# Kernel tuning notes

Measured on AMD Instinct MI355X. Metric: run time of the kernel, lower is better.

Reference implementation:

```python
import jax, jax.numpy as jnp
import numpy as np

HID = 1024
INTER = 4096
RDIM = 128          # expert_retrieval_size
HEADS = 4
NUM_EXPERTS = 16384
NUM_KEYS = 128      # sqrt(NUM_EXPERTS)
TOPK = 8            # num_cdmoe_experts_per_head
B, T = 2, 2048


def setup_inputs() -> dict:
    key = jax.random.key(0)
    ks = jax.random.split(key, 8)
    s = lambda fan_in: 1.0 / np.sqrt(fan_in)
    return {
        "hidden_states": jax.random.normal(ks[0], (B, T, HID), jnp.float32),
        "Wq": jax.random.normal(ks[1], (HEADS * RDIM, HID), jnp.float32) * s(HID),
        "keys": jax.random.normal(ks[2], (HEADS, NUM_KEYS, 2, RDIM // 2), jnp.float32) * s(RDIM // 2),
        "down_embed": jax.random.normal(ks[3], (NUM_EXPERTS, HID), jnp.float32) * 0.02,
        "up_embed": jax.random.normal(ks[4], (NUM_EXPERTS, HID), jnp.float32) * 0.02,
        "Wg": jax.random.normal(ks[5], (INTER, HID), jnp.float32) * s(HID),
        "Wu": jax.random.normal(ks[6], (INTER, HID), jnp.float32) * s(HID),
        "Wd": jax.random.normal(ks[7], (HID, INTER), jnp.float32) * s(INTER),
    }


def reference(hidden_states, Wq, keys, down_embed, up_embed, Wg, Wu, Wd):
    b, t, _ = hidden_states.shape
    # product-key retrieval
    q = hidden_states @ Wq.T                                   # [b,t,h*rdim]
    q = q.reshape(b, t, 2, HEADS, RDIM // 2)                   # [b,t,2,h,n]
    q = jnp.transpose(q, (2, 0, 1, 3, 4))                      # [2,b,t,h,n]
    sim = jnp.einsum('pbthn,hkpn->pbthk', q, keys)             # [2,b,t,h,K]
    sx, ix = jax.lax.top_k(sim[0], TOPK)                       # [b,t,h,k]
    sy, iy = jax.lax.top_k(sim[1], TOPK)
    all_scores = (sx[..., :, None] + sy[..., None, :]).reshape(b, t, HEADS, TOPK * TOPK)
    all_indices = (ix[..., :, None] * NUM_KEYS + iy[..., None, :]).reshape(b, t, HEADS, TOPK * TOPK)
    scores, pk = jax.lax.top_k(all_scores, TOPK)               # [b,t,h,k]
    indices = jnp.take_along_axis(all_indices, pk, axis=-1)    # [b,t,h,k]
    # gather expert embeddings and combine
    down = down_embed[indices]                                 # [b,t,h,k,d]
    up = up_embed[indices]                                     # [b,t,h,k,d]
    w = jnp.einsum('btd,bthkd->bthk', hidden_states, down)
    w = jax.nn.silu(w) * jax.nn.softmax(scores, axis=-1)
    experts_states = jnp.einsum('bthk,bthkd->btd', w, up)
    # dense MLP
    mlp = (jax.nn.silu(hidden_states @ Wg.T) * (hidden_states @ Wu.T)) @ Wd.T
    return mlp + experts_states
```

## Files before the change

kernel.cpp:

```cpp
#include <hip/hip_runtime.h>
#include <hip/hip_fp8.h>

#define NTOK 4096
#define HID 1024
#define QDIM 512
#define HEADS 4
#define NKEYS 128
#define TOPK 8
#define INTERDIM 4096

typedef __bf16 bf16x8 __attribute__((ext_vector_type(8)));
typedef __bf16 bf16x4 __attribute__((ext_vector_type(4)));
typedef float f32x4 __attribute__((ext_vector_type(4)));
typedef float f32x2 __attribute__((ext_vector_type(2)));

__device__ __forceinline__ float siluf(float x) { return x / (1.f + __expf(-x)); }
__device__ __forceinline__ unsigned sortable(float f) {
  unsigned u = __float_as_uint(f);
  return (u & 0x80000000u) ? ~u : (u | 0x80000000u);
}
__device__ __forceinline__ float bfl(unsigned u) { return __uint_as_float(u << 16); }
__device__ __forceinline__ float bfh(unsigned u) { return __uint_as_float(u & 0xFFFF0000u); }

__device__ __forceinline__ unsigned fp8x4_enc(float4 v) {
#if __has_builtin(__builtin_amdgcn_cvt_pk_fp8_f32)
  unsigned u = __builtin_amdgcn_cvt_pk_fp8_f32(v.x, v.y, 0, false);
  u = __builtin_amdgcn_cvt_pk_fp8_f32(v.z, v.w, u, true);
  return u;
#else
  __hip_fp8_e4m3 a(v.x), b(v.y), c(v.z), d(v.w);
  return (unsigned)a.__x | ((unsigned)b.__x << 8) | ((unsigned)c.__x << 16) | ((unsigned)d.__x << 24);
#endif
}
__device__ __forceinline__ void fp8x4_dec(unsigned u, float* o) {
#if __has_builtin(__builtin_amdgcn_cvt_pk_f32_fp8)
  f32x2 lo = __builtin_amdgcn_cvt_pk_f32_fp8(u, false);
  f32x2 hi = __builtin_amdgcn_cvt_pk_f32_fp8(u, true);
  o[0] = lo[0]; o[1] = lo[1]; o[2] = hi[0]; o[3] = hi[1];
#else
#pragma unroll
  for (int j = 0; j < 4; ++j) {
    const unsigned b = (u >> (8 * j)) & 0xFF;
    const unsigned e = (b >> 3) & 15, m = b & 7;
    float v = e ? __uint_as_float(((e + 120) << 23) | (m << 20)) : (float)m * 0x1p-9f;
    o[j] = (b & 0x80) ? -v : v;
  }
#endif
}

#define GLD_LDS16(g, l)                                                                   \
  __builtin_amdgcn_global_load_lds(                                                      \
      (const __attribute__((address_space(1))) unsigned int*)(g),                        \
      (__attribute__((address_space(3))) unsigned int*)(l), 16, 0, 0)

__device__ __forceinline__ void cast_one_f4(const float* __restrict__ src,
                                            __bf16* __restrict__ dst, int i)
{
  const float4 v = ((const float4*)src)[i];
  bf16x4 o;
  o[0] = (__bf16)v.x; o[1] = (__bf16)v.y; o[2] = (__bf16)v.z; o[3] = (__bf16)v.w;
  ((bf16x4*)dst)[i] = o;
}

__global__ __launch_bounds__(256) void cast5_kernel(
    const float* __restrict__ hs, const float* __restrict__ wq,
    const float* __restrict__ wg, const float* __restrict__ wu,
    const float* __restrict__ wd,
    __bf16* __restrict__ hs_o, __bf16* __restrict__ wq_o,
    __bf16* __restrict__ wg_o, __bf16* __restrict__ wu_o,
    __bf16* __restrict__ wd_o)
{
  int b = blockIdx.x;
  const float* src; __bf16* dst;
  if      (b < 4096)  { src = hs; dst = hs_o; }
  else if (b < 4608)  { src = wq; dst = wq_o; b -= 4096; }
  else if (b < 8704)  { src = wg; dst = wg_o; b -= 4608; }
  else if (b < 12800) { src = wu; dst = wu_o; b -= 8704; }
  else                { src = wd; dst = wd_o; b -= 12800; }
  cast_one_f4(src, dst, b * 256 + threadIdx.x);
}

__global__ __launch_bounds__(256) void cast2_kernel(
    const float* __restrict__ dwe, const float* __restrict__ upe,
    unsigned* __restrict__ dwe_o, unsigned* __restrict__ upe_o)
{
  int b = blockIdx.x;
  const float* src; unsigned* dst;
  if (b < 16384) { src = dwe; dst = dwe_o; }
  else           { src = upe; dst = upe_o; b -= 16384; }
  const int i = b * 256 + threadIdx.x;
  dst[i] = fp8x4_enc(((const float4*)src)[i]);
}

__global__ __launch_bounds__(256) void cast_keys_kernel(const float* __restrict__ keys,
                                                        __bf16* __restrict__ kbf)
{
  const int i = blockIdx.x * 256 + threadIdx.x;
  const int n = i & 63, p = (i >> 6) & 1, k = (i >> 7) & 127, h = (i >> 14) & 3;
  kbf[(((size_t)(p * 4 + h) * NKEYS) + k) * 64 + n] = (__bf16)keys[i];
}

template<bool DUAL, bool OUT_BF16>
__global__ __launch_bounds__(512) void gemm_mfma(
    const __bf16* __restrict__ A, const __bf16* __restrict__ B0,
    const __bf16* __restrict__ B1, void* __restrict__ Cv, __bf16* __restrict__ Cv1,
    int M, int N, int K, int LD, int BW, int BH, int NRX)
{
  __shared__ __attribute__((aligned(16))) __bf16 As [128 * 32];
  __shared__ __attribute__((aligned(16))) __bf16 Bs0[128 * 32];
  __shared__ __attribute__((aligned(16))) __bf16 Bs1[DUAL ? 128 * 32 : 8];

  const int bid = blockIdx.y * gridDim.x + blockIdx.x;
  const int xcd = bid & 7, idx = bid >> 3;
  const int rx = (xcd % NRX) * BW;
  const int ry = (xcd / NRX) * BH;
  const int bx = rx + idx % BW;
  const int by = ry + idx / BW;

  const int kz = blockIdx.z * K;

  const int tid  = threadIdx.x;
  const int wave = tid >> 6;
  const int lane = tid & 63;
  const int m0 = by * 128;
  const int n0 = bx * 128;
  const int wr = wave >> 2, wc = wave & 3;
  const int lhi = lane >> 4, llo = lane & 15;

  f32x4 acc0[4][2] = {};
  f32x4 acc1[4][2] = {};

  const int r0 = tid >> 2, col0 = (tid & 3) * 8;
  const __bf16* Ag  = A  + kz + (size_t)(m0 + r0) * LD + col0;
  const __bf16* B0g = B0 + kz + (size_t)(n0 + r0) * LD + col0;
  const __bf16* B1g = DUAL ? (B1 + kz + (size_t)(n0 + r0) * LD + col0) : nullptr;
  __bf16* ldsA  = &As [(size_t)wave * 512];
  __bf16* ldsB0 = &Bs0[(size_t)wave * 512];
  __bf16* ldsB1 = &Bs1[(size_t)wave * 512];

  for (int k0 = 0; k0 < K; k0 += 32) {
    GLD_LDS16(Ag  + k0, ldsA);
    GLD_LDS16(B0g + k0, ldsB0);
    if constexpr (DUAL)
      GLD_LDS16(B1g + k0, ldsB1);
    __syncthreads();

    bf16x8 afr[4], bfr0[2], bfr1[2];
#pragma unroll
    for (int mi = 0; mi < 4; ++mi)
      afr[mi] = *(const bf16x8*)&As[(wr * 64 + mi * 16 + llo) * 32 + lhi * 8];
#pragma unroll
    for (int nj = 0; nj < 2; ++nj)
      bfr0[nj] = *(const bf16x8*)&Bs0[(wc * 32 + nj * 16 + llo) * 32 + lhi * 8];
    if constexpr (DUAL) {
#pragma unroll
      for (int nj = 0; nj < 2; ++nj)
        bfr1[nj] = *(const bf16x8*)&Bs1[(wc * 32 + nj * 16 + llo) * 32 + lhi * 8];
    }
#pragma unroll
    for (int mi = 0; mi < 4; ++mi)
#pragma unroll
      for (int nj = 0; nj < 2; ++nj) {
        acc0[mi][nj] = __builtin_amdgcn_mfma_f32_16x16x32_bf16(afr[mi], bfr0[nj], acc0[mi][nj], 0, 0, 0);
        if constexpr (DUAL)
          acc1[mi][nj] = __builtin_amdgcn_mfma_f32_16x16x32_bf16(afr[mi], bfr1[nj], acc1[mi][nj], 0, 0, 0);
      }
    __syncthreads();
  }

#pragma unroll
  for (int mi = 0; mi < 4; ++mi)
#pragma unroll
    for (int nj = 0; nj < 2; ++nj)
#pragma unroll
      for (int r = 0; r < 4; ++r) {
        const int row = m0 + wr * 64 + mi * 16 + lhi * 4 + r;
        const int col = n0 + wc * 32 + nj * 16 + llo;
        float v = acc0[mi][nj][r];
        if constexpr (DUAL) v = siluf(v) * acc1[mi][nj][r];
        if constexpr (OUT_BF16) {
          ((__bf16*)Cv)[(size_t)row * N + col] = (__bf16)v;
        } else {
          if (blockIdx.z == 0) ((float*)Cv)[(size_t)row * N + col] = v;
          else Cv1[((size_t)(blockIdx.z - 1) * M + row) * N + col] = (__bf16)v;
        }
      }
}

__global__ __launch_bounds__(256) void sims_gemm(
    const __bf16* __restrict__ Qbf,
    const __bf16* __restrict__ Kbf,
    float* __restrict__ S)
{
  __shared__ __attribute__((aligned(16))) __bf16 As[128 * 32];
  __shared__ __attribute__((aligned(16))) __bf16 Bs[128 * 32];

  const int z = blockIdx.y;
  const int p = z >> 2, h = z & 3;
  const __bf16* A = Qbf + p * 256 + h * 64;
  const __bf16* B = Kbf + (size_t)z * NKEYS * 64;
  float* C = S + (size_t)z * NTOK * NKEYS;

  const int tid  = threadIdx.x;
  const int wave = tid >> 6;
  const int lane = tid & 63;
  const int m0 = blockIdx.x * 128;
  const int wr = wave >> 1, wc = wave & 1;
  const int lhi = lane >> 4, llo = lane & 15;

  f32x4 acc[4][4] = {};

  const int c0 = tid, c1 = 256 + tid;
  const int r0 = c0 >> 2, col0 = (c0 & 3) * 8;
  const int r1 = c1 >> 2, col1 = (c1 & 3) * 8;
  __bf16* ldsA0 = &As[(wave * 64) * 8];
  __bf16* ldsA1 = &As[(256 + wave * 64) * 8];
  __bf16* ldsB0 = &Bs[(wave * 64) * 8];
  __bf16* ldsB1 = &Bs[(256 + wave * 64) * 8];

  for (int k0 = 0; k0 < 64; k0 += 32) {
    GLD_LDS16(A + (size_t)(m0 + r0) * 512 + k0 + col0, ldsA0);
    GLD_LDS16(A + (size_t)(m0 + r1) * 512 + k0 + col1, ldsA1);
    GLD_LDS16(B + (size_t)r0 * 64 + k0 + col0, ldsB0);
    GLD_LDS16(B + (size_t)r1 * 64 + k0 + col1, ldsB1);
    __syncthreads();

    bf16x8 afr[4], bfr[4];
#pragma unroll
    for (int mi = 0; mi < 4; ++mi)
      afr[mi] = *(const bf16x8*)&As[(wr * 64 + mi * 16 + llo) * 32 + lhi * 8];
#pragma unroll
    for (int nj = 0; nj < 4; ++nj)
      bfr[nj] = *(const bf16x8*)&Bs[(wc * 64 + nj * 16 + llo) * 32 + lhi * 8];
#pragma unroll
    for (int mi = 0; mi < 4; ++mi)
#pragma unroll
      for (int nj = 0; nj < 4; ++nj)
        acc[mi][nj] = __builtin_amdgcn_mfma_f32_16x16x32_bf16(afr[mi], bfr[nj], acc[mi][nj], 0, 0, 0);
    __syncthreads();
  }

#pragma unroll
  for (int mi = 0; mi < 4; ++mi)
#pragma unroll
    for (int nj = 0; nj < 4; ++nj)
#pragma unroll
      for (int r = 0; r < 4; ++r) {
        const int row = m0 + wr * 64 + mi * 16 + lhi * 4 + r;
        const int col = wc * 64 + nj * 16 + llo;
        C[(size_t)row * NKEYS + col] = acc[mi][nj][r];
      }
}

__global__ __launch_bounds__(256) void topk_kernel(
    const float* __restrict__ S,
    int* __restrict__ out_idx,
    float* __restrict__ out_prob)
{
  const int g = blockIdx.x;
  const int h = blockIdx.y;
  const int t = threadIdx.x;
  const int tok0 = g * 16;

  __shared__ float    sims  [16][2][128];
  __shared__ unsigned packed[16][2][128];
  __shared__ unsigned cmax  [16][2][8];
  __shared__ int      cnt   [16][2];
  __shared__ unsigned char surv[16][2][128];
  __shared__ float    stv   [16][2][8];
  __shared__ unsigned char sti[16][2][8];
  __shared__ unsigned cnd   [16][64];

  const int ltok = t >> 4, j0 = (t & 15) * 8;
  unsigned pk[2][8];
#pragma unroll
  for (int p = 0; p < 2; ++p) {
    const float* src = S + (((size_t)(p * 4 + h) * NTOK) + tok0 + ltok) * NKEYS + j0;
    const float4 a = ((const float4*)src)[0];
    const float4 b = ((const float4*)src)[1];
    float v[8] = {a.x, a.y, a.z, a.w, b.x, b.y, b.z, b.w};
#pragma unroll
    for (int e = 0; e < 8; ++e) {
      const unsigned u = (sortable(v[e]) & 0xFFFFFF80u) | (unsigned)(127 - (j0 + e));
      sims  [ltok][p][j0 + e] = v[e];
      packed[ltok][p][j0 + e] = u;
      pk[p][e] = u;
    }
  }
  if (t < 32) cnt[t >> 1][t & 1] = 0;
  __syncthreads();

  {
    const int ctok = t >> 4, cp = (t >> 3) & 1, c = t & 7;
    const uint4* q = (const uint4*)&packed[ctok][cp][c * 16];
    unsigned m = 0;
#pragma unroll
    for (int r = 0; r < 4; ++r) {
      const uint4 u = q[r];
      m = max(m, max(max(u.x, u.y), max(u.z, u.w)));
    }
    cmax[ctok][cp][c] = m;
  }
  __syncthreads();

#pragma unroll
  for (int p = 0; p < 2; ++p) {
    const uint4* cm = (const uint4*)&cmax[ltok][p][0];
    const uint4 ca = cm[0], cb = cm[1];
    const unsigned t0 = min(min(min(ca.x, ca.y), min(ca.z, ca.w)),
                            min(min(cb.x, cb.y), min(cb.z, cb.w)));
#pragma unroll
    for (int e = 0; e < 8; ++e) {
      if (pk[p][e] >= t0) {
        const int s = atomicAdd(&cnt[ltok][p], 1);
        surv[ltok][p][s] = (unsigned char)(j0 + e);
      }
    }
  }
  __syncthreads();

  {
    const int gid = t >> 3, lane8 = t & 7;
    const int stok = gid >> 1, sp = gid & 1;
    const int n = cnt[stok][sp];
    const uint4* row = (const uint4*)&packed[stok][sp][0];
    for (int s = lane8; s < n; s += 8) {
      const int j = surv[stok][sp][s];
      const unsigned mypk = packed[stok][sp][j];
      int rk = 0;
#pragma unroll 8
      for (int q4 = 0; q4 < 32; ++q4) {
        const uint4 u = row[q4];
        rk += (u.x > mypk) + (u.y > mypk) + (u.z > mypk) + (u.w > mypk);
      }
      if (rk < TOPK) {
        stv[stok][sp][rk] = sims[stok][sp][j];
        sti[stok][sp][rk] = (unsigned char)j;
      }
    }
  }
  __syncthreads();

  const int w = t >> 6, l = t & 63;
  for (int round = 0; round < 4; ++round) {
    const int tok = w * 4 + round;
    const int ci = l >> 3, cj = l & 7;
    const float cv = stv[tok][0][ci] + stv[tok][1][cj];
    const unsigned cpk = (sortable(cv) & 0xFFFFFFC0u) | (unsigned)(63 - l);
    cnd[tok][l] = cpk;
    __syncthreads();
    int rk = 0;
    const uint4* row = (const uint4*)&cnd[tok][0];
#pragma unroll
    for (int q4 = 0; q4 < 16; ++q4) {
      const uint4 u = row[q4];
      rk += (u.x > cpk) + (u.y > cpk) + (u.z > cpk) + (u.w > cpk);
    }
    float mx = cv;
#pragma unroll
    for (int off = 32; off; off >>= 1) mx = fmaxf(mx, __shfl_xor(mx, off));
    const float e = (rk < TOPK) ? __expf(cv - mx) : 0.f;
    float sum = e;
#pragma unroll
    for (int off = 32; off; off >>= 1) sum += __shfl_xor(sum, off);
    if (rk < TOPK) {
      const int o = ((tok0 + tok) * HEADS + h) * TOPK + rk;
      out_idx [o] = (int)sti[tok][0][ci] * NKEYS + (int)sti[tok][1][cj];
      out_prob[o] = e / sum;
    }
  }
}

__device__ __forceinline__ float dotf8(const float4* h, uint4 d)
{
  float o[16];
  fp8x4_dec(d.x, o);  fp8x4_dec(d.y, o + 4);
  fp8x4_dec(d.z, o + 8); fp8x4_dec(d.w, o + 12);
  float s = 0.f;
#pragma unroll
  for (int q = 0; q < 4; ++q)
    s += h[q].x * o[4*q] + h[q].y * o[4*q+1] + h[q].z * o[4*q+2] + h[q].w * o[4*q+3];
  return s;
}

template<int NPART>
__global__ __launch_bounds__(256) void expert_kernel(
    const float* __restrict__ hs,
    const unsigned char* __restrict__ down_e,
    const unsigned char* __restrict__ up_e,
    const int* __restrict__ idx,
    const float* __restrict__ prob,
    const __bf16* __restrict__ parts,
    float* __restrict__ out)
{
  const int token = blockIdx.x;
  const int t = threadIdx.x, w = t >> 6, l = t & 63;
  __shared__ float4 sred[4][256];

  const float4* hrow = (const float4*)(hs + (size_t)token * HID);
  float4 h[4];
#pragma unroll
  for (int q = 0; q < 4; ++q) h[q] = hrow[4 * l + q];
  float acc[16] = {};

  const int*   tidx  = idx  + token * 32 + w * 8;
  const float* tprob = prob + token * 32 + w * 8;

#pragma unroll
  for (int e = 0; e < 8; e += 2) {
    const int   ex0 = tidx[e],  ex1 = tidx[e + 1];
    const float pr0 = tprob[e], pr1 = tprob[e + 1];
    const uint4 d0 = ((const uint4*)(down_e + (size_t)ex0 * HID))[l];
    const uint4 d1 = ((const uint4*)(down_e + (size_t)ex1 * HID))[l];
    const uint4 u0 = ((const uint4*)(up_e   + (size_t)ex0 * HID))[l];
    const uint4 u1 = ((const uint4*)(up_e   + (size_t)ex1 * HID))[l];

    float part0 = dotf8(h, d0);
    float part1 = dotf8(h, d1);
#pragma unroll
    for (int off = 32; off; off >>= 1) {
      part0 += __shfl_xor(part0, off);
      part1 += __shfl_xor(part1, off);
    }
    const float w0 = siluf(part0) * pr0;
    const float w1 = siluf(part1) * pr1;

    float o0[16], o1[16];
    fp8x4_dec(u0.x, o0); fp8x4_dec(u0.y, o0 + 4); fp8x4_dec(u0.z, o0 + 8); fp8x4_dec(u0.w, o0 + 12);
    fp8x4_dec(u1.x, o1); fp8x4_dec(u1.y, o1 + 4); fp8x4_dec(u1.z, o1 + 8); fp8x4_dec(u1.w, o1 + 12);
#pragma unroll
    for (int j = 0; j < 16; ++j) acc[j] += w0 * o0[j] + w1 * o1[j];
  }
#pragma unroll
  for (int q = 0; q < 4; ++q)
    sred[w][4 * l + q] = make_float4(acc[4*q], acc[4*q+1], acc[4*q+2], acc[4*q+3]);
  __syncthreads();

  const float4 r0 = sred[0][t], r1 = sred[1][t], r2 = sred[2][t], r3 = sred[3][t];
  float4* o = (float4*)(out + (size_t)token * HID);
  float4 cur = o[t];
  if constexpr (NPART > 0) {
#pragma unroll
    for (int q = 0; q < NPART; ++q) {
      const uint2 pb = ((const uint2*)(parts + ((size_t)q * NTOK + token) * HID))[t];
      cur.x += bfl(pb.x); cur.y += bfh(pb.x);
      cur.z += bfl(pb.y); cur.w += bfh(pb.y);
    }
  }
  cur.x += r0.x + r1.x + r2.x + r3.x;
  cur.y += r0.y + r1.y + r2.y + r3.y;
  cur.z += r0.z + r1.z + r2.z + r3.z;
  cur.w += r0.w + r1.w + r2.w + r3.w;
  o[t] = cur;
}

extern "C" void kernel_launch(void* const* d_in, const int* in_sizes, int n_in,
                              void* d_out, int out_size, void* d_ws, size_t ws_size,
                              hipStream_t stream)
{
  const float* hs   = (const float*)d_in[0];
  const float* Wq   = (const float*)d_in[1];
  const float* keys = (const float*)d_in[2];
  const float* dwe  = (const float*)d_in[3];
  const float* upe  = (const float*)d_in[4];
  const float* Wg   = (const float*)d_in[5];
  const float* Wu   = (const float*)d_in[6];
  const float* Wd   = (const float*)d_in[7];
  float* out = (float*)d_out;

  __bf16* qbf     = (__bf16*)d_ws;
  __bf16* kbf     = qbf + (size_t)NTOK * QDIM;
  int*    idxb    = (int*)(kbf + 8 * NKEYS * 64);
  float*  probb   = (float*)(idxb + NTOK * HEADS * TOPK);
  __bf16* hs_bf   = (__bf16*)(probb + NTOK * HEADS * TOPK);
  __bf16* wq_bf   = hs_bf + (size_t)NTOK * HID;
  __bf16* wg_bf   = wq_bf + (size_t)QDIM * HID;
  __bf16* wu_bf   = wg_bf + (size_t)INTERDIM * HID;
  __bf16* wd_bf   = wu_bf + (size_t)INTERDIM * HID;
  __bf16* interbf = wd_bf + (size_t)HID * INTERDIM;
  __bf16* parts   = interbf + (size_t)NTOK * INTERDIM;
  float*  simsb   = (float*)interbf;
  unsigned char* dwe_f8 = (unsigned char*)interbf;
  unsigned char* upe_f8 = (unsigned char*)hs_bf;

  const size_t base  = (size_t)((char*)parts - (char*)d_ws);
  const size_t psz   = (size_t)NTOK * HID * sizeof(__bf16);
  int nsplit = 1;
  if      (ws_size >= base + 3 * psz) nsplit = 4;
  else if (ws_size >= base + 1 * psz) nsplit = 2;

  cast5_kernel<<<16896, 256, 0, stream>>>(hs, Wq, Wg, Wu, Wd,
                                          hs_bf, wq_bf, wg_bf, wu_bf, wd_bf);
  cast_keys_kernel<<<256, 256, 0, stream>>>(keys, kbf);

  gemm_mfma<false, true><<<dim3(QDIM / 128, NTOK / 128), 512, 0, stream>>>(
      hs_bf, wq_bf, nullptr, qbf, nullptr, NTOK, QDIM, HID, HID, 4, 4, 1);

  sims_gemm<<<dim3(NTOK / 128, 8), 256, 0, stream>>>(qbf, kbf, simsb);
  topk_kernel<<<dim3(NTOK / 16, HEADS), 256, 0, stream>>>(simsb, idxb, probb);

  gemm_mfma<true, true><<<dim3(INTERDIM / 128, NTOK / 128), 512, 0, stream>>>(
      hs_bf, wg_bf, wu_bf, interbf, nullptr, NTOK, INTERDIM, HID, HID, 8, 16, 4);

  gemm_mfma<false, false><<<dim3(HID / 128, NTOK / 128, nsplit), 512, 0, stream>>>(
      interbf, wd_bf, nullptr, out, parts, NTOK, HID, INTERDIM / nsplit, INTERDIM, 8, 4, 1);

  cast2_kernel<<<32768, 256, 0, stream>>>(dwe, upe, (unsigned*)dwe_f8, (unsigned*)upe_f8);
  if (nsplit == 4)
    expert_kernel<3><<<NTOK, 256, 0, stream>>>(hs, dwe_f8, upe_f8, idxb, probb, parts, out);
  else if (nsplit == 2)
    expert_kernel<1><<<NTOK, 256, 0, stream>>>(hs, dwe_f8, upe_f8, idxb, probb, parts, out);
  else
    expert_kernel<0><<<NTOK, 256, 0, stream>>>(hs, dwe_f8, upe_f8, idxb, probb, nullptr, out);
}
```

Measured before the change: 287.6 us.

## Fold product keys into query weights and compute similarities in one GEMM

Precomputes WK = keys·Wq per (half, head, key) so that similarity scores come directly from hidden_states @ WK^T as a single 4096x1024x1024 GEMM. This replaces the separate query projection GEMM, the bf16 query buffer round trip, the key cast kernel and the small sims GEMM. The top-k kernel now reads scores in a token-major layout. The trade-off is a larger GEMM (N=1024 instead of 512 plus a tiny second GEMM) and a different rounding order, since the combined weights are rounded to bf16.

```diff
diff --git a/kernel.cpp b/kernel.cpp
--- a/kernel.cpp
+++ b/kernel.cpp
@@ -92,12 +92,31 @@
   dst[i] = fp8x4_enc(((const float4*)src)[i]);
 }
 
-__global__ __launch_bounds__(256) void cast_keys_kernel(const float* __restrict__ keys,
-                                                        __bf16* __restrict__ kbf)
-{
-  const int i = blockIdx.x * 256 + threadIdx.x;
-  const int n = i & 63, p = (i >> 6) & 1, k = (i >> 7) & 127, h = (i >> 14) & 3;
-  kbf[(((size_t)(p * 4 + h) * NKEYS) + k) * 64 + n] = (__bf16)keys[i];
+__global__ __launch_bounds__(256) void wk_kernel(
+    const float* __restrict__ keys,
+    const float* __restrict__ wq,
+    __bf16* __restrict__ wk)
+{
+  const int zk = blockIdx.x;
+  const int z = zk >> 7, k = zk & 127;
+  const int p = z >> 2, h = z & 3;
+  __shared__ float kv[64];
+  if (threadIdx.x < 64)
+    kv[threadIdx.x] = keys[(((size_t)(h * NKEYS + k) * 2) + p) * 64 + threadIdx.x];
+  __syncthreads();
+
+  const int d0 = threadIdx.x * 4;
+  const float* wrow = wq + (size_t)(p * 256 + h * 64) * HID + d0;
+  float acc[4] = {};
+#pragma unroll 8
+  for (int n = 0; n < 64; ++n) {
+    const float kn = kv[n];
+    const float4 w = *(const float4*)(wrow + (size_t)n * HID);
+    acc[0] += kn * w.x; acc[1] += kn * w.y; acc[2] += kn * w.z; acc[3] += kn * w.w;
+  }
+  bf16x4 o;
+  o[0] = (__bf16)acc[0]; o[1] = (__bf16)acc[1]; o[2] = (__bf16)acc[2]; o[3] = (__bf16)acc[3];
+  ((bf16x4*)(wk + (size_t)zk * HID))[threadIdx.x] = o;
 }
 
 template<bool DUAL, bool OUT_BF16>
@@ -187,71 +206,6 @@
       }
 }
 
-__global__ __launch_bounds__(256) void sims_gemm(
-    const __bf16* __restrict__ Qbf,
-    const __bf16* __restrict__ Kbf,
-    float* __restrict__ S)
-{
-  __shared__ __attribute__((aligned(16))) __bf16 As[128 * 32];
-  __shared__ __attribute__((aligned(16))) __bf16 Bs[128 * 32];
-
-  const int z = blockIdx.y;
-  const int p = z >> 2, h = z & 3;
-  const __bf16* A = Qbf + p * 256 + h * 64;
-  const __bf16* B = Kbf + (size_t)z * NKEYS * 64;
-  float* C = S + (size_t)z * NTOK * NKEYS;
-
-  const int tid  = threadIdx.x;
-  const int wave = tid >> 6;
-  const int lane = tid & 63;
-  const int m0 = blockIdx.x * 128;
-  const int wr = wave >> 1, wc = wave & 1;
-  const int lhi = lane >> 4, llo = lane & 15;
-
-  f32x4 acc[4][4] = {};
-
-  const int c0 = tid, c1 = 256 + tid;
-  const int r0 = c0 >> 2, col0 = (c0 & 3) * 8;
-  const int r1 = c1 >> 2, col1 = (c1 & 3) * 8;
-  __bf16* ldsA0 = &As[(wave * 64) * 8];
-  __bf16* ldsA1 = &As[(256 + wave * 64) * 8];
-  __bf16* ldsB0 = &Bs[(wave * 64) * 8];
-  __bf16* ldsB1 = &Bs[(256 + wave * 64) * 8];
-
-  for (int k0 = 0; k0 < 64; k0 += 32) {
-    GLD_LDS16(A + (size_t)(m0 + r0) * 512 + k0 + col0, ldsA0);
-    GLD_LDS16(A + (size_t)(m0 + r1) * 512 + k0 + col1, ldsA1);
-    GLD_LDS16(B + (size_t)r0 * 64 + k0 + col0, ldsB0);
-    GLD_LDS16(B + (size_t)r1 * 64 + k0 + col1, ldsB1);
-    __syncthreads();
-
-    bf16x8 afr[4], bfr[4];
-#pragma unroll
-    for (int mi = 0; mi < 4; ++mi)
-      afr[mi] = *(const bf16x8*)&As[(wr * 64 + mi * 16 + llo) * 32 + lhi * 8];
-#pragma unroll
-    for (int nj = 0; nj < 4; ++nj)
-      bfr[nj] = *(const bf16x8*)&Bs[(wc * 64 + nj * 16 + llo) * 32 + lhi * 8];
-#pragma unroll
-    for (int mi = 0; mi < 4; ++mi)
-#pragma unroll
-      for (int nj = 0; nj < 4; ++nj)
-        acc[mi][nj] = __builtin_amdgcn_mfma_f32_16x16x32_bf16(afr[mi], bfr[nj], acc[mi][nj], 0, 0, 0);
-    __syncthreads();
-  }
-
-#pragma unroll
-  for (int mi = 0; mi < 4; ++mi)
-#pragma unroll
-    for (int nj = 0; nj < 4; ++nj)
-#pragma unroll
-      for (int r = 0; r < 4; ++r) {
-        const int row = m0 + wr * 64 + mi * 16 + lhi * 4 + r;
-        const int col = wc * 64 + nj * 16 + llo;
-        C[(size_t)row * NKEYS + col] = acc[mi][nj][r];
-      }
-}
-
 __global__ __launch_bounds__(256) void topk_kernel(
     const float* __restrict__ S,
     int* __restrict__ out_idx,
@@ -275,7 +229,7 @@
   unsigned pk[2][8];
 #pragma unroll
   for (int p = 0; p < 2; ++p) {
-    const float* src = S + (((size_t)(p * 4 + h) * NTOK) + tok0 + ltok) * NKEYS + j0;
+    const float* src = S + (size_t)(tok0 + ltok) * 1024 + (p * 4 + h) * 128 + j0;
     const float4 a = ((const float4*)src)[0];
     const float4 b = ((const float4*)src)[1];
     float v[8] = {a.x, a.y, a.z, a.w, b.x, b.y, b.z, b.w};
@@ -468,9 +422,8 @@
   const float* Wd   = (const float*)d_in[7];
   float* out = (float*)d_out;
 
-  __bf16* qbf     = (__bf16*)d_ws;
-  __bf16* kbf     = qbf + (size_t)NTOK * QDIM;
-  int*    idxb    = (int*)(kbf + 8 * NKEYS * 64);
+  __bf16* wkbf    = (__bf16*)d_ws;
+  int*    idxb    = (int*)(wkbf + (size_t)8 * NKEYS * HID);
   float*  probb   = (float*)(idxb + NTOK * HEADS * TOPK);
   __bf16* hs_bf   = (__bf16*)(probb + NTOK * HEADS * TOPK);
   __bf16* wq_bf   = hs_bf + (size_t)NTOK * HID;
@@ -491,12 +444,11 @@
 
   cast5_kernel<<<16896, 256, 0, stream>>>(hs, Wq, Wg, Wu, Wd,
                                           hs_bf, wq_bf, wg_bf, wu_bf, wd_bf);
-  cast_keys_kernel<<<256, 256, 0, stream>>>(keys, kbf);
-
-  gemm_mfma<false, true><<<dim3(QDIM / 128, NTOK / 128), 512, 0, stream>>>(
-      hs_bf, wq_bf, nullptr, qbf, nullptr, NTOK, QDIM, HID, HID, 4, 4, 1);
-
-  sims_gemm<<<dim3(NTOK / 128, 8), 256, 0, stream>>>(qbf, kbf, simsb);
+  wk_kernel<<<8 * NKEYS, 256, 0, stream>>>(keys, Wq, wkbf);
+
+  gemm_mfma<false, false><<<dim3(8, NTOK / 128), 512, 0, stream>>>(
+      hs_bf, wkbf, nullptr, simsb, nullptr, NTOK, 1024, HID, HID, 8, 4, 1);
+
   topk_kernel<<<dim3(NTOK / 16, HEADS), 256, 0, stream>>>(simsb, idxb, probb);
 
   gemm_mfma<true, true><<<dim3(INTERDIM / 128, NTOK / 128), 512, 0, stream>>>(
```

Result: no change. 293.1 us (+1.9%).
